# Optimization experiments

Measured on AMD Instinct MI355X. Metric: run time of the kernel, lower is better.

The kernel has to match this reference:

```python
import jax, jax.numpy as jnp
import numpy as np

T, B, E, H = 200, 2048, 256, 512
P0, P1, NC = 256, 128, 1
ALPHA = 0.3  # keras LeakyReLU default


def _predict(h, W0, b0, W1, b1, Wf, bf):
    # Dense -> LeakyReLU -> (dropout=identity) x2, then sigmoid(Dense)
    h = jax.nn.leaky_relu(h @ W0 + b0, ALPHA)
    h = jax.nn.leaky_relu(h @ W1 + b1, ALPHA)
    return jax.nn.sigmoid(h @ Wf + bf)  # [B, 1]


def setup_inputs() -> dict:
    key = jax.random.key(0)
    ks = jax.random.split(key, 24)
    s = 0.05  # keras 'random_normal' initializer stddev
    d = {
        "inputs": jax.random.normal(ks[0], (T, B, E), jnp.float32),
        # gate order along leading axis: f, i, o, g
        "Wx_c": s * jax.random.normal(ks[1], (4, E, H), jnp.float32),
        "bx_c": jnp.zeros((4, H), jnp.float32),
        "Wh_c": s * jax.random.normal(ks[2], (4, H, H), jnp.float32),
        "Wx_v": s * jax.random.normal(ks[3], (4, E, H), jnp.float32),
        "bx_v": jnp.zeros((4, H), jnp.float32),
        "Wh_v": s * jax.random.normal(ks[4], (4, H, H), jnp.float32),
        # order: s_c_hat_c, s_c_hat_v, s_v_hat_v, s_v_hat_c
        "Ws": s * jax.random.normal(ks[5], (4, H, H), jnp.float32),
        "Wpc0": s * jax.random.normal(ks[6], (H, P0), jnp.float32),
        "bpc0": jnp.zeros((P0,), jnp.float32),
        "Wpc1": s * jax.random.normal(ks[7], (P0, P1), jnp.float32),
        "bpc1": jnp.zeros((P1,), jnp.float32),
        "Wfcc": s * jax.random.normal(ks[8], (P1, NC), jnp.float32),
        "bfcc": jnp.zeros((NC,), jnp.float32),
        "Wpv0": s * jax.random.normal(ks[9], (H, P0), jnp.float32),
        "bpv0": jnp.zeros((P0,), jnp.float32),
        "Wpv1": s * jax.random.normal(ks[10], (P0, P1), jnp.float32),
        "bpv1": jnp.zeros((P1,), jnp.float32),
        "Wfcv": s * jax.random.normal(ks[11], (P1, NC), jnp.float32),
        "bfcv": jnp.zeros((NC,), jnp.float32),
    }
    return d


def reference(inputs, Wx_c, bx_c, Wh_c, Wx_v, bx_v, Wh_v, Ws,
              Wpc0, bpc0, Wpc1, bpc1, Wfcc, bfcc,
              Wpv0, bpv0, Wpv1, bpv1, Wfcv, bfcv):
    batch = inputs.shape[1]
    zeros = jnp.zeros((batch, H), inputs.dtype)
    # initial g = predict_c(H_c=0), broadcast in place of tf.tile(g,[1,n_hidden])
    g0 = _predict(zeros, Wpc0, bpc0, Wpc1, bpc1, Wfcc, bfcc)  # [B,1]
    ones1 = jnp.ones_like(g0)

    def step(carry, x):
        H_c, H_v, s_c, s_v, g, pc, pv = carry
        # click stream gates: f,i,o,g fused along leading axis
        gx = jnp.einsum('be,keh->kbh', x, Wx_c) + bx_c[:, None, :]
        gh = jnp.einsum('bh,khg->kbg', H_c, Wh_c)
        pre = gx + gh
        f_c, i_c, o_c = jax.nn.sigmoid(pre[0]), jax.nn.sigmoid(pre[1]), jax.nn.sigmoid(pre[2])
        g_c = jnp.tanh(pre[3])
        s_c_hat = jnp.tanh((1.0 - g) * (H_c @ Ws[0]) + g * (H_v @ Ws[1]))
        s_c = s_c_hat + i_c * g_c + (1.0 - g) * (f_c * s_c)
        H_c = o_c * jnp.tanh(s_c)
        H_c_p = _predict(H_c, Wpc0, bpc0, Wpc1, bpc1, Wfcc, bfcc)  # [B,1]
        # no click_label branch: g = H_c_p
        g = H_c_p
        pc = jnp.where(H_c_p >= 0.5, ones1, (1.0 - H_c_p) * pc)
        # conversion stream gates (driven by updated H_c)
        gxv = jnp.einsum('be,keh->kbh', x, Wx_v) + bx_v[:, None, :]
        ghv = jnp.einsum('bh,khg->kbg', H_c, Wh_v)
        prev = gxv + ghv
        f_v, i_v, o_v = jax.nn.sigmoid(prev[0]), jax.nn.sigmoid(prev[1]), jax.nn.sigmoid(prev[2])
        g_v = jnp.tanh(prev[3])
        s_v_hat = jnp.tanh(H_v @ Ws[2] + g * (H_c @ Ws[3]))
        s_v = s_v_hat + (1.0 - g) * s_v + g * (f_v * s_v + i_v * g_v)
        H_v = (1.0 - g) * H_v + g * (o_v * jnp.tanh(s_v))
        H_v_p = _predict(H_v, Wpv0, bpv0, Wpv1, bpv1, Wfcv, bfcv) * H_c_p
        pv = jnp.where(H_c_p >= 0.5, ones1, (1.0 - H_v_p) * pv)
        return (H_c, H_v, s_c, s_v, g, pc, pv), (H_c_p, H_v_p)

    carry0 = (zeros, zeros, zeros, zeros, g0, ones1, ones1)
    _, (pred_c, pred_v) = jax.lax.scan(step, carry0, inputs)
    return pred_c, pred_v  # each [T, B, 1]
```

## Files before the change

kernel.cpp:

```cpp
#include <hip/hip_runtime.h>
#include <cstdint>
#include <cstddef>

constexpr int T_STEPS = 200;
constexpr int BATCH   = 2048;
constexpr int E_DIM   = 256;
constexpr int H_DIM   = 512;
constexpr int P0_DIM  = 256;
constexpr int P1_DIM  = 128;
constexpr float ALPHA = 0.3f;

typedef __attribute__((ext_vector_type(8))) _Float16 f16x8;
typedef __attribute__((ext_vector_type(4))) float f32x4;

__device__ __forceinline__ float sigmoidf_(float x){ return 1.0f/(1.0f+expf(-x)); }

__device__ __forceinline__ unsigned short f2h(float f){
    union { _Float16 h; unsigned short u; } v;
    v.h = (_Float16)f;
    return v.u;
}

#define GLOAD16(gp, lp) __builtin_amdgcn_global_load_lds( \
    (const __attribute__((address_space(1))) unsigned int*)(gp), \
    (__attribute__((address_space(3))) unsigned int*)(lp), 16, 0, 0)

template<int ROWS>
__device__ __forceinline__ void stage64(const unsigned short* __restrict__ src, int ldk,
                                        char* ldsbase){
    constexpr int TOT = ROWS * 8;
    const int tid = threadIdx.x;
#pragma unroll
    for (int i = 0; i < TOT/256; ++i){
        const int gsl = i*256 + tid;
        const int r = gsl >> 3, s = gsl & 7;
        const int ksrc = ((s ^ (r & 7)) << 3);
        GLOAD16(src + (size_t)r*ldk + ksrc, ldsbase + gsl*16);
    }
}

__device__ __forceinline__ f16x8 ldsfragh(const char* ldsbase, int row, int kslot){
    return *(const f16x8*)(ldsbase + row*128 + ((kslot ^ (row & 7)) << 4));
}

template<bool HAS_B1, bool HAS_B2, int KSLABS>
__device__ __forceinline__ void fused_phase(
    const unsigned short* __restrict__ A, int lda,
    const unsigned short* __restrict__ B1,
    const unsigned short* __restrict__ B2,
    f32x4 (&accg)[2][4], f32x4 (&acce)[2],
    char* lds, int wr, int wc, int lr, int lq)
{
    stage64<64>(A, lda, lds);
    if (HAS_B1) stage64<128>(B1, 768, lds + 8192);
    if (HAS_B2) stage64<32>(B2, 512, lds + 24576);
    int cur = 0;
    for (int s = 0; s < KSLABS; ++s){
        char* bufc = lds + cur*32768;
        if (s + 1 < KSLABS){
            char* bufn = lds + (cur^1)*32768;
            stage64<64>(A + (s+1)*64, lda, bufn);
            if (HAS_B1) stage64<128>(B1 + (s+1)*64, 768, bufn + 8192);
            if (HAS_B2) stage64<32>(B2 + (s+1)*64, 512, bufn + 24576);
            if constexpr (HAS_B1 && HAS_B2)
                asm volatile("s_waitcnt vmcnt(7)" ::: "memory");
            else if constexpr (HAS_B1)
                asm volatile("s_waitcnt vmcnt(6)" ::: "memory");
            else
                asm volatile("s_waitcnt vmcnt(3)" ::: "memory");
        } else {
            asm volatile("s_waitcnt vmcnt(0)" ::: "memory");
        }
        __builtin_amdgcn_s_barrier();
        __builtin_amdgcn_sched_barrier(0);
        __builtin_amdgcn_s_setprio(1);
#pragma unroll
        for (int kk = 0; kk < 2; ++kk){
            f16x8 a[2];
#pragma unroll
            for (int m = 0; m < 2; ++m) a[m] = ldsfragh(bufc, wr*32 + m*16 + lr, kk*4 + lq);
            if (HAS_B1){
#pragma unroll
                for (int n = 0; n < 4; ++n){
                    f16x8 b = ldsfragh(bufc + 8192, wc*64 + n*16 + lr, kk*4 + lq);
#pragma unroll
                    for (int m = 0; m < 2; ++m)
                        accg[m][n] = __builtin_amdgcn_mfma_f32_16x16x32_f16(a[m], b, accg[m][n], 0,0,0);
                }
            }
            if (HAS_B2){
                f16x8 b = ldsfragh(bufc + 24576, wc*16 + lr, kk*4 + lq);
#pragma unroll
                for (int m = 0; m < 2; ++m)
                    acce[m] = __builtin_amdgcn_mfma_f32_16x16x32_f16(a[m], b, acce[m], 0,0,0);
            }
        }
        __builtin_amdgcn_s_setprio(0);
        __builtin_amdgcn_sched_barrier(0);
        __builtin_amdgcn_s_barrier();
        cur ^= 1;
    }
}

__global__ __launch_bounds__(256, 2) void k_fused(
    const unsigned short* __restrict__ Xh,
    const unsigned short* __restrict__ AH,
    const unsigned short* __restrict__ AV,
    const unsigned short* __restrict__ WT2,
    const float* __restrict__ bias,
    const unsigned short* __restrict__ WsH,
    const unsigned short* __restrict__ WsV,
    const float* __restrict__ g,
    float* __restrict__ sstate, float* __restrict__ Hv32,
    unsigned short* __restrict__ Hnew,
    const int mode)
{
    __shared__ __align__(16) char lds[65536];
    const int tid = threadIdx.x;
    const int lane = tid & 63, wid = tid >> 6;
    const int wr = wid >> 1, wc = wid & 1;
    const int lr = lane & 15, lq = lane >> 4;

    const int id = blockIdx.x;
    const int virt = ((id & 7) << 6) | (id >> 3);
    const int hgrp = virt >> 5;
    const int brow = (virt & 31) * 64;
    const int h0   = hgrp * 32;

    f32x4 accg[2][4], acceH[2], acceV[2];
#pragma unroll
    for (int m = 0; m < 2; ++m){
        f32x4 z = {0.f,0.f,0.f,0.f};
#pragma unroll
        for (int n = 0; n < 4; ++n) accg[m][n] = z;
        acceH[m] = z; acceV[m] = z;
    }

    const unsigned short* WTp = WT2 + (size_t)hgrp*128*768;
    fused_phase<true,false,4>(Xh + (size_t)brow*E_DIM, E_DIM, WTp, nullptr,
                              accg, acceH, lds, wr, wc, lr, lq);
    fused_phase<true,true,8>(AH + (size_t)brow*H_DIM, H_DIM, WTp + E_DIM,
                             WsH + (size_t)h0*H_DIM,
                             accg, acceH, lds, wr, wc, lr, lq);
    fused_phase<false,true,8>(AV + (size_t)brow*H_DIM, H_DIM, nullptr,
                              WsV + (size_t)h0*H_DIM,
                              accg, acceV, lds, wr, wc, lr, lq);

    float* ldsG  = (float*)lds;
    float* ldsEH = (float*)(lds + 33792);
    float* ldsEV = (float*)(lds + 42240);
#pragma unroll
    for (int m = 0; m < 2; ++m){
#pragma unroll
        for (int n = 0; n < 4; ++n){
            const int col = wc*64 + n*16 + lr;
            const int z = col >> 5, hl = col & 31;
            const float bs = bias[z*H_DIM + h0 + hl];
#pragma unroll
            for (int r = 0; r < 4; ++r){
                const int row = wr*32 + m*16 + lq*4 + r;
                float v = accg[m][n][r] + bs;
                v = (z < 3) ? sigmoidf_(v) : tanhf(v);
                ldsG[row*132 + col] = v;
            }
        }
    }
#pragma unroll
    for (int m = 0; m < 2; ++m){
        const int col = wc*16 + lr;
#pragma unroll
        for (int r = 0; r < 4; ++r){
            const int row = wr*32 + m*16 + lq*4 + r;
            ldsEH[row*33 + col] = acceH[m][r];
            ldsEV[row*33 + col] = acceV[m][r];
        }
    }
    __syncthreads();

    const int crow = tid >> 2, ch = (tid & 3) * 8;
    const int grow = brow + crow;
    const float gv = g[grow];
    const size_t gbase = (size_t)grow*H_DIM + h0 + ch;
    union U4 { float4 v; float s[4]; };
    U4 sv0, sv1, hv0, hv1;
    sv0.v = *(const float4*)&sstate[gbase];
    sv1.v = *(const float4*)&sstate[gbase + 4];
    if (mode == 1){
        hv0.v = *(const float4*)&Hv32[gbase];
        hv1.v = *(const float4*)&Hv32[gbase + 4];
    }
    U4 sn0, sn1, hn0, hn1;
    union { unsigned short u[8]; f16x8 v; } hh;
#pragma unroll
    for (int e = 0; e < 8; ++e){
        const int hc = ch + e;
        const float f_ = ldsG[crow*132 + hc];
        const float i_ = ldsG[crow*132 + 32 + hc];
        const float o_ = ldsG[crow*132 + 64 + hc];
        const float q_ = ldsG[crow*132 + 96 + hc];
        const float eh = ldsEH[crow*33 + hc];
        const float ev = ldsEV[crow*33 + hc];
        const float a1 = (mode == 0) ? eh : ev;
        const float a2 = (mode == 0) ? ev : eh;
        const float svo = (e < 4) ? sv0.s[e] : sv1.s[e-4];
        float s, hval;
        if (mode == 0){
            const float shat = tanhf((1.0f - gv)*a1 + gv*a2);
            s = shat + i_*q_ + (1.0f - gv)*(f_*svo);
            hval = o_ * tanhf(s);
        } else {
            const float shat = tanhf(a1 + gv*a2);
            s = shat + (1.0f - gv)*svo + gv*(f_*svo + i_*q_);
            const float hvo = (e < 4) ? hv0.s[e] : hv1.s[e-4];
            hval = (1.0f - gv)*hvo + gv*(o_*tanhf(s));
            if (e < 4) hn0.s[e] = hval; else hn1.s[e-4] = hval;
        }
        if (e < 4) sn0.s[e] = s; else sn1.s[e-4] = s;
        hh.u[e] = f2h(hval);
    }
    *(float4*)&sstate[gbase]     = sn0.v;
    *(float4*)&sstate[gbase + 4] = sn1.v;
    if (mode == 1){
        *(float4*)&Hv32[gbase]     = hn0.v;
        *(float4*)&Hv32[gbase + 4] = hn1.v;
    }
    *(f16x8*)&Hnew[gbase] = hh.v;
}

__device__ __forceinline__ void predict_dev(
    int pblk, const unsigned short* __restrict__ Hh,
    const unsigned short* __restrict__ W0T, const float* __restrict__ b0,
    const unsigned short* __restrict__ W1T, const float* __restrict__ b1,
    const float* __restrict__ Wf, const float* __restrict__ bf_,
    float* gstate, const float* __restrict__ gmul, float* pred, char* lds)
{
    char*  ldsA = lds;
    char*  ldsB = lds + 4096;
    char*  ldsP = lds + 36864;
    float* sums = (float*)(lds + 53248);
    const int tid = threadIdx.x, lane = tid & 63, w = tid >> 6;
    const int lr = lane & 15, lq = lane >> 4;
    const int brow = pblk * 32;

    f32x4 acc0[2][4];
#pragma unroll
    for (int m = 0; m < 2; ++m)
#pragma unroll
        for (int n = 0; n < 4; ++n){ f32x4 z = {0.f,0.f,0.f,0.f}; acc0[m][n] = z; }

    for (int k0 = 0; k0 < H_DIM; k0 += 64){
        stage64<32>(Hh + (size_t)brow*H_DIM + k0, H_DIM, ldsA);
        stage64<256>(W0T + k0, H_DIM, ldsB);
        __syncthreads();
#pragma unroll
        for (int kk = 0; kk < 2; ++kk){
            f16x8 a[2], b[4];
#pragma unroll
            for (int m = 0; m < 2; ++m) a[m] = ldsfragh(ldsA, m*16 + lr, kk*4 + lq);
#pragma unroll
            for (int n = 0; n < 4; ++n) b[n] = ldsfragh(ldsB, w*64 + n*16 + lr, kk*4 + lq);
#pragma unroll
            for (int m = 0; m < 2; ++m)
#pragma unroll
                for (int n = 0; n < 4; ++n)
                    acc0[m][n] = __builtin_amdgcn_mfma_f32_16x16x32_f16(a[m], b[n], acc0[m][n], 0,0,0);
        }
        __syncthreads();
    }
#pragma unroll
    for (int m = 0; m < 2; ++m){
#pragma unroll
        for (int n = 0; n < 4; ++n){
            const int col = w*64 + n*16 + lr;
            const float bs = b0[col];
#pragma unroll
            for (int r = 0; r < 4; ++r){
                const int row = m*16 + lq*4 + r;
                float x = acc0[m][n][r] + bs;
                x = (x > 0.0f) ? x : ALPHA*x;
                *(unsigned short*)(ldsP + row*512 + ((((col >> 3)) ^ (row & 7)) << 4) + (col & 7)*2) = f2h(x);
            }
        }
    }
    __syncthreads();

    f32x4 accp[2][2];
#pragma unroll
    for (int m = 0; m < 2; ++m)
#pragma unroll
        for (int n = 0; n < 2; ++n){ f32x4 z = {0.f,0.f,0.f,0.f}; accp[m][n] = z; }

    for (int k0 = 0; k0 < P0_DIM; k0 += 64){
        stage64<128>(W1T + k0, P0_DIM, ldsB);
        __syncthreads();
#pragma unroll
        for (int kk = 0; kk < 2; ++kk){
            f16x8 a[2], b[2];
#pragma unroll
            for (int m = 0; m < 2; ++m){
                const int row = m*16 + lr;
                const int slot = (k0 >> 3) + kk*4 + lq;
                a[m] = *(const f16x8*)(ldsP + row*512 + ((slot ^ (row & 7)) << 4));
            }
#pragma unroll
            for (int n = 0; n < 2; ++n) b[n] = ldsfragh(ldsB, w*32 + n*16 + lr, kk*4 + lq);
#pragma unroll
            for (int m = 0; m < 2; ++m)
#pragma unroll
                for (int n = 0; n < 2; ++n)
                    accp[m][n] = __builtin_amdgcn_mfma_f32_16x16x32_f16(a[m], b[n], accp[m][n], 0,0,0);
        }
        __syncthreads();
    }

    float part[8];
#pragma unroll
    for (int j = 0; j < 8; ++j) part[j] = 0.0f;
#pragma unroll
    for (int m = 0; m < 2; ++m){
#pragma unroll
        for (int n = 0; n < 2; ++n){
            const int col = w*32 + n*16 + lr;
            const float bs = b1[col], wf = Wf[col];
#pragma unroll
            for (int r = 0; r < 4; ++r){
                float x = accp[m][n][r] + bs;
                x = (x > 0.0f) ? x : ALPHA*x;
                part[m*4 + r] += x * wf;
            }
        }
    }
#pragma unroll
    for (int mask = 1; mask < 16; mask <<= 1)
#pragma unroll
        for (int j = 0; j < 8; ++j) part[j] += __shfl_xor(part[j], mask);
    if (lr == 0){
#pragma unroll
        for (int j = 0; j < 8; ++j){
            const int row = (j >> 2)*16 + lq*4 + (j & 3);
            sums[w*32 + row] = part[j];
        }
    }
    __syncthreads();
    if (tid < 32){
        float tot = sums[tid] + sums[32 + tid] + sums[64 + tid] + sums[96 + tid] + bf_[0];
        float val = sigmoidf_(tot);
        const int rowg = brow + tid;
        if (gmul)   val *= gmul[rowg];
        if (gstate) gstate[rowg] = val;
        if (pred)   pred[rowg]   = val;
    }
}

__device__ __forceinline__ void xcvt_dev(int blk, const float* __restrict__ x,
                                         unsigned short* __restrict__ oh)
{
    const int tid = threadIdx.x;
#pragma unroll
    for (int j = 0; j < 4; ++j){
        const int t = blk*256 + tid + j*32768;
        float4 v = ((const float4*)x)[t];
        ushort4 h;
        h.x = f2h(v.x); h.y = f2h(v.y); h.z = f2h(v.z); h.w = f2h(v.w);
        ((ushort4*)oh)[t] = h;
    }
}

__global__ __launch_bounds__(256) void k_LB(
    const unsigned short* __restrict__ Hcn,
    const unsigned short* __restrict__ Wp0Tc, const float* __restrict__ bpc0,
    const unsigned short* __restrict__ Wp1Tc, const float* __restrict__ bpc1,
    const float* __restrict__ Wfcc, const float* __restrict__ bfcc,
    float* __restrict__ gnew, float* __restrict__ predc,
    const unsigned short* __restrict__ Hvb,
    const unsigned short* __restrict__ Wp0Tv, const float* __restrict__ bpv0,
    const unsigned short* __restrict__ Wp1Tv, const float* __restrict__ bpv1,
    const float* __restrict__ Wfcv, const float* __restrict__ bfcv,
    const float* __restrict__ gold, float* __restrict__ predv,
    const float* __restrict__ xnext, unsigned short* __restrict__ Xnh)
{
    __shared__ __align__(16) char lds[53760];
    const int id = blockIdx.x;
    if (id < 64){
        predict_dev(id, Hcn, Wp0Tc, bpc0, Wp1Tc, bpc1, Wfcc, bfcc,
                    gnew, nullptr, predc, lds);
    } else if (id < 128){
        if (predv) predict_dev(id - 64, Hvb, Wp0Tv, bpv0, Wp1Tv, bpv1, Wfcv, bfcv,
                               nullptr, gold, predv, lds);
    } else {
        if (Xnh) xcvt_dev(id - 128, xnext, Xnh);
    }
}

__global__ __launch_bounds__(256) void k_predict_g(
    const unsigned short* __restrict__ Hh,
    const unsigned short* __restrict__ W0T, const float* __restrict__ b0,
    const unsigned short* __restrict__ W1T, const float* __restrict__ b1,
    const float* __restrict__ Wf, const float* __restrict__ bf_,
    float* gstate, const float* __restrict__ gmul, float* pred)
{
    __shared__ __align__(16) char lds[53760];
    predict_dev(blockIdx.x, Hh, W0T, b0, W1T, b1, Wf, bf_, gstate, gmul, pred, lds);
}

__global__ __launch_bounds__(256) void k_xcvt_g(const float* __restrict__ x,
                                                unsigned short* __restrict__ oh)
{
    xcvt_dev(blockIdx.x, x, oh);
}

__global__ __launch_bounds__(256) void k_wcat(const float* __restrict__ Wx,
                                              const float* __restrict__ Wh,
                                              unsigned short* __restrict__ oh){
    const int n = blockIdx.y;
    const int k = blockIdx.x*256 + threadIdx.x;
    const int z = (n >> 5) & 3;
    const int h = ((n >> 7) << 5) | (n & 31);
    float v = (k < 256) ? Wx[((size_t)z*E_DIM + k)*H_DIM + h]
                        : Wh[((size_t)z*H_DIM + (k - 256))*H_DIM + h];
    oh[(size_t)n*768 + k] = f2h(v);
}

__global__ __launch_bounds__(256) void k_trans(const float* __restrict__ in,
                                               unsigned short* __restrict__ oh,
                                               int K, int N){
    const int k = blockIdx.x*256 + threadIdx.x;
    const int n = blockIdx.y;
    if (k < K) oh[(size_t)n*K + k] = f2h(in[(size_t)k*N + n]);
}

__global__ __launch_bounds__(256) void k_init(float* __restrict__ sc, float* __restrict__ sv,
                                              float* __restrict__ hv32,
                                              unsigned short* __restrict__ hc0,
                                              unsigned short* __restrict__ hv0){
    const int i = blockIdx.x*256 + threadIdx.x;
    sc[i] = 0.0f; sv[i] = 0.0f; hv32[i] = 0.0f;
    hc0[i] = 0; hv0[i] = 0;
}

extern "C" void kernel_launch(void* const* d_in, const int* in_sizes, int n_in,
                              void* d_out, int out_size, void* d_ws, size_t ws_size,
                              hipStream_t stream)
{
    (void)in_sizes; (void)n_in; (void)out_size; (void)ws_size;

    const float* inputs = (const float*)d_in[0];
    const float* Wx_c   = (const float*)d_in[1];
    const float* bx_c   = (const float*)d_in[2];
    const float* Wh_c   = (const float*)d_in[3];
    const float* Wx_v   = (const float*)d_in[4];
    const float* bx_v   = (const float*)d_in[5];
    const float* Wh_v   = (const float*)d_in[6];
    const float* Ws     = (const float*)d_in[7];
    const float* Wpc0   = (const float*)d_in[8];
    const float* bpc0   = (const float*)d_in[9];
    const float* Wpc1   = (const float*)d_in[10];
    const float* bpc1   = (const float*)d_in[11];
    const float* Wfcc   = (const float*)d_in[12];
    const float* bfcc   = (const float*)d_in[13];
    const float* Wpv0   = (const float*)d_in[14];
    const float* bpv0   = (const float*)d_in[15];
    const float* Wpv1   = (const float*)d_in[16];
    const float* bpv1   = (const float*)d_in[17];
    const float* Wfcv   = (const float*)d_in[18];
    const float* bfcv   = (const float*)d_in[19];
    float* out = (float*)d_out;

    char* ws = (char*)d_ws;
    size_t off = 0;
    auto allocB = [&](size_t bytes) -> char* {
        char* p = ws + off;
        off = (off + bytes + 255) & ~(size_t)255;
        return p;
    };
    const size_t BH = (size_t)BATCH * H_DIM;
    const size_t BE = (size_t)BATCH * E_DIM;

    unsigned short* Xh[2];
    Xh[0] = (unsigned short*)allocB(BE*2);
    Xh[1] = (unsigned short*)allocB(BE*2);
    unsigned short* WT2c  = (unsigned short*)allocB((size_t)2048*768*2);
    unsigned short* WT2v  = (unsigned short*)allocB((size_t)2048*768*2);
    unsigned short* WsT   = (unsigned short*)allocB((size_t)4*H_DIM*H_DIM*2);
    unsigned short* Wp0Tc = (unsigned short*)allocB((size_t)P0_DIM*H_DIM*2);
    unsigned short* Wp0Tv = (unsigned short*)allocB((size_t)P0_DIM*H_DIM*2);
    unsigned short* Wp1Tc = (unsigned short*)allocB((size_t)P1_DIM*P0_DIM*2);
    unsigned short* Wp1Tv = (unsigned short*)allocB((size_t)P1_DIM*P0_DIM*2);
    unsigned short* Hc[2], *Hv[2];
    Hc[0] = (unsigned short*)allocB(BH*2);
    Hc[1] = (unsigned short*)allocB(BH*2);
    Hv[0] = (unsigned short*)allocB(BH*2);
    Hv[1] = (unsigned short*)allocB(BH*2);
    float* sc    = (float*)allocB(BH*4);
    float* sv    = (float*)allocB(BH*4);
    float* hv32  = (float*)allocB(BH*4);
    float* gbuf[2];
    gbuf[0] = (float*)allocB(BATCH*4);
    gbuf[1] = (float*)allocB(BATCH*4);

    const dim3 thr(256);
    const size_t HH = (size_t)H_DIM * H_DIM;

    k_wcat<<<dim3(3, 2048), thr, 0, stream>>>(Wx_c, Wh_c, WT2c);
    k_wcat<<<dim3(3, 2048), thr, 0, stream>>>(Wx_v, Wh_v, WT2v);
    for (int i = 0; i < 4; ++i)
        k_trans<<<dim3(2, 512), thr, 0, stream>>>(Ws + i*HH, WsT + i*HH, H_DIM, H_DIM);
    k_trans<<<dim3(2, 256), thr, 0, stream>>>(Wpc0, Wp0Tc, H_DIM, P0_DIM);
    k_trans<<<dim3(2, 256), thr, 0, stream>>>(Wpv0, Wp0Tv, H_DIM, P0_DIM);
    k_trans<<<dim3(1, 128), thr, 0, stream>>>(Wpc1, Wp1Tc, P0_DIM, P1_DIM);
    k_trans<<<dim3(1, 128), thr, 0, stream>>>(Wpv1, Wp1Tv, P0_DIM, P1_DIM);

    k_init<<<4096, thr, 0, stream>>>(sc, sv, hv32, Hc[0], Hv[0]);
    k_predict_g<<<64, thr, 0, stream>>>(Hc[0], Wp0Tc, bpc0, Wp1Tc, bpc1, Wfcc, bfcc,
                                        gbuf[0], nullptr, nullptr);
    k_xcvt_g<<<128, thr, 0, stream>>>(inputs, Xh[0]);

    for (int t = 0; t < T_STEPS; ++t){
        const int cur = t & 1, nxt = cur ^ 1;

        k_fused<<<512, thr, 0, stream>>>(Xh[cur], Hc[cur], Hv[cur],
                                         WT2c, bx_c,
                                         WsT + 0*HH,
                                         WsT + 1*HH,
                                         gbuf[cur], sc, nullptr, Hc[nxt], 0);

        k_LB<<<256, thr, 0, stream>>>(Hc[nxt], Wp0Tc, bpc0, Wp1Tc, bpc1, Wfcc, bfcc,
                                      gbuf[nxt], out + (size_t)t*BATCH,
                                      Hv[cur], Wp0Tv, bpv0, Wp1Tv, bpv1, Wfcv, bfcv,
                                      gbuf[cur],
                                      (t > 0) ? out + (size_t)(T_STEPS + t - 1)*BATCH
                                              : nullptr,
                                      inputs + (size_t)(t+1)*BE,
                                      (t + 1 < T_STEPS) ? Xh[nxt] : nullptr);

        k_fused<<<512, thr, 0, stream>>>(Xh[cur], Hc[nxt], Hv[cur],
                                         WT2v, bx_v,
                                         WsT + 3*HH,
                                         WsT + 2*HH,
                                         gbuf[nxt], sv, hv32, Hv[nxt], 1);
    }
    k_predict_g<<<64, thr, 0, stream>>>(Hv[0], Wp0Tv, bpv0, Wp1Tv, bpv1, Wfcv, bfcv,
                                        nullptr, gbuf[0],
                                        out + (size_t)(2*T_STEPS - 1)*BATCH);
}
```

Before: 10.47 ms.

## Double k_fused batch tile to 128 rows per block for weight reuse

Each k_fused block now covers 128 batch rows instead of 64. Each wave computes 4 M-fragments, so every staged weight tile feeds twice as many MFMAs, and the grid shrinks from 512 to 256 blocks. The larger LDS buffer and accumulator set drop occupancy to one block per CU, and the epilogue is split into two 64-row phases that reuse the LDS scratch. This halves redundant weight traffic per step, at the cost of fewer resident waves to hide latency and only 256 blocks, roughly one per CU on a 256-CU part.

```diff
diff --git a/kernel.cpp b/kernel.cpp
--- a/kernel.cpp
+++ b/kernel.cpp
@@ -48,26 +48,26 @@
     const unsigned short* __restrict__ A, int lda,
     const unsigned short* __restrict__ B1,
     const unsigned short* __restrict__ B2,
-    f32x4 (&accg)[2][4], f32x4 (&acce)[2],
+    f32x4 (&accg)[4][4], f32x4 (&acce)[4],
     char* lds, int wr, int wc, int lr, int lq)
 {
-    stage64<64>(A, lda, lds);
-    if (HAS_B1) stage64<128>(B1, 768, lds + 8192);
-    if (HAS_B2) stage64<32>(B2, 512, lds + 24576);
+    stage64<128>(A, lda, lds);
+    if (HAS_B1) stage64<128>(B1, 768, lds + 16384);
+    if (HAS_B2) stage64<32>(B2, 512, lds + 32768);
     int cur = 0;
     for (int s = 0; s < KSLABS; ++s){
-        char* bufc = lds + cur*32768;
+        char* bufc = lds + cur*36864;
         if (s + 1 < KSLABS){
-            char* bufn = lds + (cur^1)*32768;
-            stage64<64>(A + (s+1)*64, lda, bufn);
-            if (HAS_B1) stage64<128>(B1 + (s+1)*64, 768, bufn + 8192);
-            if (HAS_B2) stage64<32>(B2 + (s+1)*64, 512, bufn + 24576);
+            char* bufn = lds + (cur^1)*36864;
+            stage64<128>(A + (s+1)*64, lda, bufn);
+            if (HAS_B1) stage64<128>(B1 + (s+1)*64, 768, bufn + 16384);
+            if (HAS_B2) stage64<32>(B2 + (s+1)*64, 512, bufn + 32768);
             if constexpr (HAS_B1 && HAS_B2)
-                asm volatile("s_waitcnt vmcnt(7)" ::: "memory");
+                asm volatile("s_waitcnt vmcnt(9)" ::: "memory");
             else if constexpr (HAS_B1)
-                asm volatile("s_waitcnt vmcnt(6)" ::: "memory");
+                asm volatile("s_waitcnt vmcnt(8)" ::: "memory");
             else
-                asm volatile("s_waitcnt vmcnt(3)" ::: "memory");
+                asm volatile("s_waitcnt vmcnt(5)" ::: "memory");
         } else {
             asm volatile("s_waitcnt vmcnt(0)" ::: "memory");
         }
@@ -76,23 +76,23 @@
         __builtin_amdgcn_s_setprio(1);
 #pragma unroll
         for (int kk = 0; kk < 2; ++kk){
-            f16x8 a[2];
-#pragma unroll
-            for (int m = 0; m < 2; ++m) a[m] = ldsfragh(bufc, wr*32 + m*16 + lr, kk*4 + lq);
+            f16x8 a[4];
+#pragma unroll
+            for (int m = 0; m < 4; ++m) a[m] = ldsfragh(bufc, wr*64 + m*16 + lr, kk*4 + lq);
             if (HAS_B1){
 #pragma unroll
                 for (int n = 0; n < 4; ++n){
-                    f16x8 b = ldsfragh(bufc + 8192, wc*64 + n*16 + lr, kk*4 + lq);
-#pragma unroll
-                    for (int m = 0; m < 2; ++m)
+                    f16x8 b = ldsfragh(bufc + 16384, wc*64 + n*16 + lr, kk*4 + lq);
+#pragma unroll
+                    for (int m = 0; m < 4; ++m)
                         accg[m][n] = __builtin_amdgcn_mfma_f32_16x16x32_f16(a[m], b, accg[m][n], 0,0,0);
                 }
             }
             if (HAS_B2){
-                f16x8 b = ldsfragh(bufc + 24576, wc*16 + lr, kk*4 + lq);
-#pragma unroll
-                for (int m = 0; m < 2; ++m)
-                    acce[m] = __builtin_amdgcn_mfma_f32_16x16x32_f16(a[m], b, acce[m], 0,0,0);
+                f16x8 bx = ldsfragh(bufc + 32768, wc*16 + lr, kk*4 + lq);
+#pragma unroll
+                for (int m = 0; m < 4; ++m)
+                    acce[m] = __builtin_amdgcn_mfma_f32_16x16x32_f16(a[m], bx, acce[m], 0,0,0);
             }
         }
         __builtin_amdgcn_s_setprio(0);
@@ -102,7 +102,7 @@
     }
 }
 
-__global__ __launch_bounds__(256, 2) void k_fused(
+__global__ __launch_bounds__(256, 1) void k_fused(
     const unsigned short* __restrict__ Xh,
     const unsigned short* __restrict__ AH,
     const unsigned short* __restrict__ AV,
@@ -115,21 +115,21 @@
     unsigned short* __restrict__ Hnew,
     const int mode)
 {
-    __shared__ __align__(16) char lds[65536];
+    __shared__ __align__(16) char lds[73728];
     const int tid = threadIdx.x;
     const int lane = tid & 63, wid = tid >> 6;
     const int wr = wid >> 1, wc = wid & 1;
     const int lr = lane & 15, lq = lane >> 4;
 
     const int id = blockIdx.x;
-    const int virt = ((id & 7) << 6) | (id >> 3);
-    const int hgrp = virt >> 5;
-    const int brow = (virt & 31) * 64;
+    const int virt = ((id & 7) << 5) | (id >> 3);
+    const int hgrp = virt >> 4;
+    const int brow = (virt & 15) * 128;
     const int h0   = hgrp * 32;
 
-    f32x4 accg[2][4], acceH[2], acceV[2];
-#pragma unroll
-    for (int m = 0; m < 2; ++m){
+    f32x4 accg[4][4], acceH[4], acceV[4];
+#pragma unroll
+    for (int m = 0; m < 4; ++m){
         f32x4 z = {0.f,0.f,0.f,0.f};
 #pragma unroll
         for (int n = 0; n < 4; ++n) accg[m][n] = z;
@@ -149,82 +149,84 @@
     float* ldsG  = (float*)lds;
     float* ldsEH = (float*)(lds + 33792);
     float* ldsEV = (float*)(lds + 42240);
-#pragma unroll
-    for (int m = 0; m < 2; ++m){
-#pragma unroll
-        for (int n = 0; n < 4; ++n){
-            const int col = wc*64 + n*16 + lr;
-            const int z = col >> 5, hl = col & 31;
-            const float bs = bias[z*H_DIM + h0 + hl];
-#pragma unroll
-            for (int r = 0; r < 4; ++r){
-                const int row = wr*32 + m*16 + lq*4 + r;
-                float v = accg[m][n][r] + bs;
-                v = (z < 3) ? sigmoidf_(v) : tanhf(v);
-                ldsG[row*132 + col] = v;
-            }
-        }
-    }
-#pragma unroll
-    for (int m = 0; m < 2; ++m){
-        const int col = wc*16 + lr;
-#pragma unroll
-        for (int r = 0; r < 4; ++r){
-            const int row = wr*32 + m*16 + lq*4 + r;
-            ldsEH[row*33 + col] = acceH[m][r];
-            ldsEV[row*33 + col] = acceV[m][r];
-        }
-    }
-    __syncthreads();
-
-    const int crow = tid >> 2, ch = (tid & 3) * 8;
-    const int grow = brow + crow;
-    const float gv = g[grow];
-    const size_t gbase = (size_t)grow*H_DIM + h0 + ch;
-    union U4 { float4 v; float s[4]; };
-    U4 sv0, sv1, hv0, hv1;
-    sv0.v = *(const float4*)&sstate[gbase];
-    sv1.v = *(const float4*)&sstate[gbase + 4];
-    if (mode == 1){
-        hv0.v = *(const float4*)&Hv32[gbase];
-        hv1.v = *(const float4*)&Hv32[gbase + 4];
-    }
-    U4 sn0, sn1, hn0, hn1;
-    union { unsigned short u[8]; f16x8 v; } hh;
-#pragma unroll
-    for (int e = 0; e < 8; ++e){
-        const int hc = ch + e;
-        const float f_ = ldsG[crow*132 + hc];
-        const float i_ = ldsG[crow*132 + 32 + hc];
-        const float o_ = ldsG[crow*132 + 64 + hc];
-        const float q_ = ldsG[crow*132 + 96 + hc];
-        const float eh = ldsEH[crow*33 + hc];
-        const float ev = ldsEV[crow*33 + hc];
-        const float a1 = (mode == 0) ? eh : ev;
-        const float a2 = (mode == 0) ? ev : eh;
-        const float svo = (e < 4) ? sv0.s[e] : sv1.s[e-4];
-        float s, hval;
-        if (mode == 0){
-            const float shat = tanhf((1.0f - gv)*a1 + gv*a2);
-            s = shat + i_*q_ + (1.0f - gv)*(f_*svo);
-            hval = o_ * tanhf(s);
-        } else {
-            const float shat = tanhf(a1 + gv*a2);
-            s = shat + (1.0f - gv)*svo + gv*(f_*svo + i_*q_);
-            const float hvo = (e < 4) ? hv0.s[e] : hv1.s[e-4];
-            hval = (1.0f - gv)*hvo + gv*(o_*tanhf(s));
-            if (e < 4) hn0.s[e] = hval; else hn1.s[e-4] = hval;
-        }
-        if (e < 4) sn0.s[e] = s; else sn1.s[e-4] = s;
-        hh.u[e] = f2h(hval);
-    }
-    *(float4*)&sstate[gbase]     = sn0.v;
-    *(float4*)&sstate[gbase + 4] = sn1.v;
-    if (mode == 1){
-        *(float4*)&Hv32[gbase]     = hn0.v;
-        *(float4*)&Hv32[gbase + 4] = hn1.v;
-    }
-    *(f16x8*)&Hnew[gbase] = hh.v;
+    for (int ph = 0; ph < 2; ++ph){
+        __syncthreads();
+        if (wr == ph){
+#pragma unroll
+            for (int m = 0; m < 4; ++m){
+#pragma unroll
+                for (int n = 0; n < 4; ++n){
+                    const int col = wc*64 + n*16 + lr;
+                    const int z = col >> 5, hl = col & 31;
+                    const float bs = bias[z*H_DIM + h0 + hl];
+#pragma unroll
+                    for (int r = 0; r < 4; ++r){
+                        const int rowl = m*16 + lq*4 + r;
+                        float v = accg[m][n][r] + bs;
+                        v = (z < 3) ? sigmoidf_(v) : tanhf(v);
+                        ldsG[rowl*132 + col] = v;
+                    }
+                }
+                const int col2 = wc*16 + lr;
+#pragma unroll
+                for (int r = 0; r < 4; ++r){
+                    const int rowl = m*16 + lq*4 + r;
+                    ldsEH[rowl*33 + col2] = acceH[m][r];
+                    ldsEV[rowl*33 + col2] = acceV[m][r];
+                }
+            }
+        }
+        __syncthreads();
+
+        const int crow = tid >> 2, lqq = tid & 3, ch = lqq * 8;
+        const int grow = brow + ph*64 + crow;
+        const float gv = g[grow];
+        const size_t gbase = (size_t)grow*H_DIM + h0 + ch;
+        union U4 { float4 v; float s[4]; };
+        U4 sv0, sv1, hv0, hv1;
+        sv0.v = *(const float4*)&sstate[gbase];
+        sv1.v = *(const float4*)&sstate[gbase + 4];
+        if (mode == 1){
+            hv0.v = *(const float4*)&Hv32[gbase];
+            hv1.v = *(const float4*)&Hv32[gbase + 4];
+        }
+        U4 sn0, sn1, hn0, hn1;
+        union { unsigned short u[8]; f16x8 v; } hu;
+#pragma unroll
+        for (int e = 0; e < 8; ++e){
+            const int hc = ch + e;
+            const float f_ = ldsG[crow*132 + hc];
+            const float i_ = ldsG[crow*132 + 32 + hc];
+            const float o_ = ldsG[crow*132 + 64 + hc];
+            const float q_ = ldsG[crow*132 + 96 + hc];
+            const float eh = ldsEH[crow*33 + hc];
+            const float ev = ldsEV[crow*33 + hc];
+            const float a1 = (mode == 0) ? eh : ev;
+            const float a2 = (mode == 0) ? ev : eh;
+            const float svo = (e < 4) ? sv0.s[e] : sv1.s[e-4];
+            float s, hval;
+            if (mode == 0){
+                const float shat = tanhf((1.0f - gv)*a1 + gv*a2);
+                s = shat + i_*q_ + (1.0f - gv)*(f_*svo);
+                hval = o_ * tanhf(s);
+            } else {
+                const float shat = tanhf(a1 + gv*a2);
+                s = shat + (1.0f - gv)*svo + gv*(f_*svo + i_*q_);
+                const float hvo = (e < 4) ? hv0.s[e] : hv1.s[e-4];
+                hval = (1.0f - gv)*hvo + gv*(o_*tanhf(s));
+                if (e < 4) hn0.s[e] = hval; else hn1.s[e-4] = hval;
+            }
+            if (e < 4) sn0.s[e] = s; else sn1.s[e-4] = s;
+            hu.u[e] = f2h(hval);
+        }
+        *(float4*)&sstate[gbase]     = sn0.v;
+        *(float4*)&sstate[gbase + 4] = sn1.v;
+        if (mode == 1){
+            *(float4*)&Hv32[gbase]     = hn0.v;
+            *(float4*)&Hv32[gbase + 4] = hn1.v;
+        }
+        *(f16x8*)&Hnew[gbase] = hu.v;
+    }
 }
 
 __device__ __forceinline__ void predict_dev(
@@ -518,7 +520,7 @@
     for (int t = 0; t < T_STEPS; ++t){
         const int cur = t & 1, nxt = cur ^ 1;
 
-        k_fused<<<512, thr, 0, stream>>>(Xh[cur], Hc[cur], Hv[cur],
+        k_fused<<<256, thr, 0, stream>>>(Xh[cur], Hc[cur], Hv[cur],
                                          WT2c, bx_c,
                                          WsT + 0*HH,
                                          WsT + 1*HH,
@@ -533,7 +535,7 @@
                                       inputs + (size_t)(t+1)*BE,
                                       (t + 1 < T_STEPS) ? Xh[nxt] : nullptr);
 
-        k_fused<<<512, thr, 0, stream>>>(Xh[cur], Hc[nxt], Hv[cur],
+        k_fused<<<256, thr, 0, stream>>>(Xh[cur], Hc[nxt], Hv[cur],
                                          WT2v, bx_v,
                                          WsT + 3*HH,
                                          WsT + 2*HH,
```

Measured after the change: 14.72 ms. 40.6% more time.

## Double-buffer LDS staging in predict MLP GEMMs to overlap loads with MFMA

Applied to the files above, without the earlier changes.

Converts both K-loops in predict_dev from single-buffer staging with two __syncthreads per step to ping-pong LDS buffers. The next chunk is prefetched with global_load_lds while the current one feeds the MFMAs, and explicit vmcnt waits plus s_barrier replace full syncs. This aims to hide global-load latency in the small per-timestep predict kernels. LDS grows to about 90KB per block, which lowers occupancy, and correctness depends on the hand-set vmcnt counts matching the number of loads stage64 issues.

```diff
diff --git a/kernel.cpp b/kernel.cpp
--- a/kernel.cpp
+++ b/kernel.cpp
@@ -234,10 +234,8 @@
     const float* __restrict__ Wf, const float* __restrict__ bf_,
     float* gstate, const float* __restrict__ gmul, float* pred, char* lds)
 {
-    char*  ldsA = lds;
-    char*  ldsB = lds + 4096;
-    char*  ldsP = lds + 36864;
-    float* sums = (float*)(lds + 53248);
+    char*  ldsP = lds + 73728;
+    float* sums = (float*)(lds + 90112);
     const int tid = threadIdx.x, lane = tid & 63, w = tid >> 6;
     const int lr = lane & 15, lq = lane >> 4;
     const int brow = pblk * 32;
@@ -248,25 +246,39 @@
 #pragma unroll
         for (int n = 0; n < 4; ++n){ f32x4 z = {0.f,0.f,0.f,0.f}; acc0[m][n] = z; }
 
-    for (int k0 = 0; k0 < H_DIM; k0 += 64){
-        stage64<32>(Hh + (size_t)brow*H_DIM + k0, H_DIM, ldsA);
-        stage64<256>(W0T + k0, H_DIM, ldsB);
-        __syncthreads();
+    stage64<32>(Hh + (size_t)brow*H_DIM, H_DIM, lds);
+    stage64<256>(W0T, H_DIM, lds + 4096);
+    int cur = 0;
+    for (int s = 0; s < 8; ++s){
+        char* bufc = lds + cur*36864;
+        if (s + 1 < 8){
+            char* bufn = lds + (cur^1)*36864;
+            stage64<32>(Hh + (size_t)brow*H_DIM + (s+1)*64, H_DIM, bufn);
+            stage64<256>(W0T + (s+1)*64, H_DIM, bufn + 4096);
+            asm volatile("s_waitcnt vmcnt(9)" ::: "memory");
+        } else {
+            asm volatile("s_waitcnt vmcnt(0)" ::: "memory");
+        }
+        __builtin_amdgcn_s_barrier();
+        __builtin_amdgcn_sched_barrier(0);
 #pragma unroll
         for (int kk = 0; kk < 2; ++kk){
             f16x8 a[2], b[4];
 #pragma unroll
-            for (int m = 0; m < 2; ++m) a[m] = ldsfragh(ldsA, m*16 + lr, kk*4 + lq);
-#pragma unroll
-            for (int n = 0; n < 4; ++n) b[n] = ldsfragh(ldsB, w*64 + n*16 + lr, kk*4 + lq);
+            for (int m = 0; m < 2; ++m) a[m] = ldsfragh(bufc, m*16 + lr, kk*4 + lq);
+#pragma unroll
+            for (int n = 0; n < 4; ++n) b[n] = ldsfragh(bufc + 4096, w*64 + n*16 + lr, kk*4 + lq);
 #pragma unroll
             for (int m = 0; m < 2; ++m)
 #pragma unroll
                 for (int n = 0; n < 4; ++n)
                     acc0[m][n] = __builtin_amdgcn_mfma_f32_16x16x32_f16(a[m], b[n], acc0[m][n], 0,0,0);
         }
-        __syncthreads();
-    }
+        __builtin_amdgcn_sched_barrier(0);
+        __builtin_amdgcn_s_barrier();
+        cur ^= 1;
+    }
+
 #pragma unroll
     for (int m = 0; m < 2; ++m){
 #pragma unroll
@@ -290,27 +302,39 @@
 #pragma unroll
         for (int n = 0; n < 2; ++n){ f32x4 z = {0.f,0.f,0.f,0.f}; accp[m][n] = z; }
 
-    for (int k0 = 0; k0 < P0_DIM; k0 += 64){
-        stage64<128>(W1T + k0, P0_DIM, ldsB);
-        __syncthreads();
+    stage64<128>(W1T, P0_DIM, lds + 4096);
+    cur = 0;
+    for (int s = 0; s < 4; ++s){
+        char* bufc = lds + cur*36864;
+        if (s + 1 < 4){
+            char* bufn = lds + (cur^1)*36864;
+            stage64<128>(W1T + (s+1)*64, P0_DIM, bufn + 4096);
+            asm volatile("s_waitcnt vmcnt(4)" ::: "memory");
+        } else {
+            asm volatile("s_waitcnt vmcnt(0)" ::: "memory");
+        }
+        __builtin_amdgcn_s_barrier();
+        __builtin_amdgcn_sched_barrier(0);
 #pragma unroll
         for (int kk = 0; kk < 2; ++kk){
             f16x8 a[2], b[2];
 #pragma unroll
             for (int m = 0; m < 2; ++m){
                 const int row = m*16 + lr;
-                const int slot = (k0 >> 3) + kk*4 + lq;
+                const int slot = s*8 + kk*4 + lq;
                 a[m] = *(const f16x8*)(ldsP + row*512 + ((slot ^ (row & 7)) << 4));
             }
 #pragma unroll
-            for (int n = 0; n < 2; ++n) b[n] = ldsfragh(ldsB, w*32 + n*16 + lr, kk*4 + lq);
+            for (int n = 0; n < 2; ++n) b[n] = ldsfragh(bufc + 4096, w*32 + n*16 + lr, kk*4 + lq);
 #pragma unroll
             for (int m = 0; m < 2; ++m)
 #pragma unroll
                 for (int n = 0; n < 2; ++n)
                     accp[m][n] = __builtin_amdgcn_mfma_f32_16x16x32_f16(a[m], b[n], accp[m][n], 0,0,0);
         }
-        __syncthreads();
+        __builtin_amdgcn_sched_barrier(0);
+        __builtin_amdgcn_s_barrier();
+        cur ^= 1;
     }
 
     float part[8];
@@ -379,7 +403,7 @@
     const float* __restrict__ gold, float* __restrict__ predv,
     const float* __restrict__ xnext, unsigned short* __restrict__ Xnh)
 {
-    __shared__ __align__(16) char lds[53760];
+    __shared__ __align__(16) char lds[90624];
     const int id = blockIdx.x;
     if (id < 64){
         predict_dev(id, Hcn, Wp0Tc, bpc0, Wp1Tc, bpc1, Wfcc, bfcc,
@@ -399,7 +423,7 @@
     const float* __restrict__ Wf, const float* __restrict__ bf_,
     float* gstate, const float* __restrict__ gmul, float* pred)
 {
-    __shared__ __align__(16) char lds[53760];
+    __shared__ __align__(16) char lds[90624];
     predict_dev(blockIdx.x, Hh, W0T, b0, W1T, b1, Wf, bf_, gstate, gmul, pred, lds);
 }
 
```

Measured after the change: 9.832 ms. 6.1% less time.
